# Kernel optimization log

Hardware: AMD Instinct MI355X
Metric: run time of the kernel (lower is better)

## Reference

```python
import jax, jax.numpy as jnp
import numpy as np

N, MUL, NUM_ELEM = 2048, 128, 10
D_IN = 9                      # single-copy input irreps 0e+1o+2e -> 1+3+5
IN_DIMS = (1, 3, 5)           # per-irrep dims of irreps_in
OUT_DIMS = (1, 3)             # per-irrep dims of irreps_out (0e, 1o)
OUT_SLICES = ((0, 1), (1, 4)) # slices into per-mul output of width 4
# (nu, out_idx, n_basis) entries, mirroring reduced_symmetric_tensor_product_basis
ENTRIES = ((1, 0, 1), (1, 1, 1), (2, 0, 3), (2, 1, 2), (3, 0, 4), (3, 1, 2))


def setup_inputs() -> dict:
    key = jax.random.key(0)
    ks = jax.random.split(key, 2 + 2 * len(ENTRIES))
    inp = {}
    inp["node_feats"] = jax.random.normal(ks[0], (N, MUL * D_IN), dtype=jnp.float32)
    inp["species"] = jax.random.randint(ks[1], (N,), 0, NUM_ELEM)
    for i, (nu, oi, nb) in enumerate(ENTRIES):
        d = OUT_DIMS[oi]
        inp[f"basis{i}"] = jax.random.normal(ks[2 + 2 * i], (D_IN,) * nu + (nb, d), dtype=jnp.float32)
        inp[f"weight{i}"] = jax.random.normal(ks[3 + 2 * i], (NUM_ELEM, nb, MUL), dtype=jnp.float32) * (1.0 / np.sqrt(nb))
    return inp


def _to_per_mul(x):
    # (N, sum mul*dim) -> (N, mul, 9)
    pieces, off = [], 0
    for d in IN_DIMS:
        pieces.append(x[:, off:off + MUL * d].reshape(-1, MUL, d))
        off += MUL * d
    return jnp.concatenate(pieces, axis=-1)


def _from_per_mul(x):
    # (N, mul, 4) -> (N, mul*1 + mul*3)
    pieces = []
    for oi, d in enumerate(OUT_DIMS):
        lo, hi = OUT_SLICES[oi]
        pieces.append(x[:, :, lo:hi].reshape(-1, MUL * d))
    return jnp.concatenate(pieces, axis=-1)


def _forward(node_feats, bases, weights, species):
    feats = _to_per_mul(node_feats)                         # (N, mul, 9)
    out = jnp.zeros((feats.shape[0], MUL, 4), dtype=feats.dtype)
    for i, (nu, oi, nb) in enumerate(ENTRIES):
        basis = jax.lax.stop_gradient(bases[i]).astype(feats.dtype)
        tmp = jnp.einsum('a...,nma->nm...', basis, feats)   # (N, mul, 9^(nu-1), nb, d)
        for _ in range(nu - 1):
            tmp = jnp.einsum('nma...,nma->nm...', tmp, feats)
        w = weights[i][species]                             # (N, nb, mul) per-species gather
        contracted = jnp.einsum('nsm,nmsp->nmp', w, tmp)    # (N, mul, d)
        lo, hi = OUT_SLICES[oi]
        out = out.at[:, :, lo:hi].add(contracted)
    return _from_per_mul(out)


def reference(node_feats, species, basis0, weight0, basis1, weight1, basis2, weight2,
              basis3, weight3, basis4, weight4, basis5, weight5):
    bases = [basis0, basis1, basis2, basis3, basis4, basis5]
    weights = [weight0, weight1, weight2, weight3, weight4, weight5]
    return _forward(node_feats, bases, weights, species)
```

## Files before the change

kernel.cpp:

```cpp
#include <hip/hip_runtime.h>


#define N_NODES 2048
#define MUL     128
#define NROW    1152
#define NQ      45
#define NC      165
#define Q4_BASE 12
#define C4_BASE 147
#define S4_TOTAL 642

__global__ void k_prep(const float* __restrict__ b0, const float* __restrict__ b1,
                       const float* __restrict__ b2, const float* __restrict__ b3,
                       const float* __restrict__ b4, const float* __restrict__ b5,
                       float4* __restrict__ S) {
    const int t = threadIdx.x;
    if (t < 9) {
        S[t] = make_float4(b0[t], b1[t * 3 + 0], b1[t * 3 + 1], b1[t * 3 + 2]);
    } else if (t < Q4_BASE) {
        S[t] = make_float4(0.f, 0.f, 0.f, 0.f);
    } else if (t < Q4_BASE + NQ) {
        const int k = t - Q4_BASE;
        int a = -1, b = -1, kk = k;
        for (int aa = 0; aa < 9 && a < 0; ++aa) {
            const int cnt = 9 - aa;
            if (kk < cnt) { a = aa; b = aa + kk; } else kk -= cnt;
        }
        const float mult = (a == b) ? 0.5f : 1.0f;
        const int i1 = a * 9 + b, i2 = b * 9 + a;
        float s2[3], s3[6];
        for (int s = 0; s < 3; ++s)
            s2[s] = (b2[i1 * 3 + s] + b2[i2 * 3 + s]) * mult;
        for (int s = 0; s < 2; ++s)
            for (int d = 0; d < 3; ++d)
                s3[s * 3 + d] = (b3[(i1 * 2 + s) * 3 + d] + b3[(i2 * 2 + s) * 3 + d]) * mult;
        S[Q4_BASE + k * 3 + 0] = make_float4(s2[0], s2[1], s2[2], 0.f);
        S[Q4_BASE + k * 3 + 1] = make_float4(s3[0], s3[1], s3[2], s3[3]);
        S[Q4_BASE + k * 3 + 2] = make_float4(s3[4], s3[5], 0.f, 0.f);
    } else if (t < Q4_BASE + NQ + NC) {
        const int k = t - Q4_BASE - NQ;
        int a = -1, b = -1, c = -1, kk = k;
        for (int aa = 0; aa < 9 && a < 0; ++aa)
            for (int bb = aa; bb < 9 && a < 0; ++bb) {
                const int cnt = 9 - bb;
                if (kk < cnt) { a = aa; b = bb; c = bb + kk; } else kk -= cnt;
            }
        const float mult = (a == b && b == c) ? (1.0f / 6.0f)
                         : ((a == b || b == c) ? 0.5f : 1.0f);
        int p[6];
        p[0] = (a * 9 + b) * 9 + c;  p[1] = (a * 9 + c) * 9 + b;
        p[2] = (b * 9 + a) * 9 + c;  p[3] = (b * 9 + c) * 9 + a;
        p[4] = (c * 9 + a) * 9 + b;  p[5] = (c * 9 + b) * 9 + a;
        float s4[4], s5[6];
        for (int s = 0; s < 4; ++s) {
            float v = 0.f;
            for (int j = 0; j < 6; ++j) v += b4[p[j] * 4 + s];
            s4[s] = v * mult;
        }
        for (int s = 0; s < 2; ++s)
            for (int d = 0; d < 3; ++d) {
                float v = 0.f;
                for (int j = 0; j < 6; ++j) v += b5[(p[j] * 2 + s) * 3 + d];
                s5[s * 3 + d] = v * mult;
            }
        S[C4_BASE + k * 3 + 0] = make_float4(s4[0], s4[1], s4[2], s4[3]);
        S[C4_BASE + k * 3 + 1] = make_float4(s5[0], s5[1], s5[2], s5[3]);
        S[C4_BASE + k * 3 + 2] = make_float4(s5[4], s5[5], 0.f, 0.f);
    }
}

__global__ __launch_bounds__(256) void k_eval(
        const float* __restrict__ nf, const int* __restrict__ species,
        const float* __restrict__ w0, const float* __restrict__ w1,
        const float* __restrict__ w2, const float* __restrict__ w3,
        const float* __restrict__ w4, const float* __restrict__ w5,
        const float4* __restrict__ Sg, float* __restrict__ out) {
    __shared__ float4 S[S4_TOTAL];
    const int tid = threadIdx.x;
    for (int i = tid; i < S4_TOTAL; i += 256) S[i] = Sg[i];
    __syncthreads();

    const int m = tid & 127;
    const int nbase = blockIdx.x * 4 + (tid >> 7) * 2;

    float f[2][9];
    float wv0[2], wv1[2], wv2[2][3], wv3[2][2], wv4[2][4], wv5[2][2];
#pragma unroll
    for (int i = 0; i < 2; ++i) {
        const int n = nbase + i;
        const float* __restrict__ row = nf + (size_t)n * NROW;
        f[i][0] = row[m];
#pragma unroll
        for (int j = 0; j < 3; ++j) f[i][1 + j] = row[128 + 3 * m + j];
#pragma unroll
        for (int j = 0; j < 5; ++j) f[i][4 + j] = row[512 + 5 * m + j];
        const int e = species[n];
        wv0[i] = w0[e * MUL + m];
        wv1[i] = w1[e * MUL + m];
#pragma unroll
        for (int s = 0; s < 3; ++s) wv2[i][s] = w2[(e * 3 + s) * MUL + m];
#pragma unroll
        for (int s = 0; s < 2; ++s) wv3[i][s] = w3[(e * 2 + s) * MUL + m];
#pragma unroll
        for (int s = 0; s < 4; ++s) wv4[i][s] = w4[(e * 4 + s) * MUL + m];
#pragma unroll
        for (int s = 0; s < 2; ++s) wv5[i][s] = w5[(e * 2 + s) * MUL + m];
    }

    float A0[2] = {0.f, 0.f};
    float A1[2][3] = {};
    float B2[2][3] = {}, B3[2][6] = {};
    float B4[2][4] = {}, B5[2][6] = {};

#pragma unroll
    for (int a = 0; a < 9; ++a) {
        const float4 L = S[a];
#pragma unroll
        for (int i = 0; i < 2; ++i) {
            A0[i]    += L.x * f[i][a];
            A1[i][0] += L.y * f[i][a];
            A1[i][1] += L.z * f[i][a];
            A1[i][2] += L.w * f[i][a];
        }
    }

    int kq = 0, kc = 0;
#pragma unroll
    for (int a = 0; a < 9; ++a) {
#pragma unroll
        for (int b = a; b < 9; ++b) {
            float q[2];
            q[0] = f[0][a] * f[0][b];
            q[1] = f[1][a] * f[1][b];
            {
                const float4 r0 = S[Q4_BASE + kq * 3 + 0];
                const float4 r1 = S[Q4_BASE + kq * 3 + 1];
                const float4 r2 = S[Q4_BASE + kq * 3 + 2];
#pragma unroll
                for (int i = 0; i < 2; ++i) {
                    B2[i][0] += q[i] * r0.x; B2[i][1] += q[i] * r0.y; B2[i][2] += q[i] * r0.z;
                    B3[i][0] += q[i] * r1.x; B3[i][1] += q[i] * r1.y; B3[i][2] += q[i] * r1.z;
                    B3[i][3] += q[i] * r1.w; B3[i][4] += q[i] * r2.x; B3[i][5] += q[i] * r2.y;
                }
                ++kq;
            }
#pragma unroll
            for (int c = b; c < 9; ++c) {
                const float4 r0 = S[C4_BASE + kc * 3 + 0];
                const float4 r1 = S[C4_BASE + kc * 3 + 1];
                const float4 r2 = S[C4_BASE + kc * 3 + 2];
#pragma unroll
                for (int i = 0; i < 2; ++i) {
                    const float tt = q[i] * f[i][c];
                    B4[i][0] += tt * r0.x; B4[i][1] += tt * r0.y;
                    B4[i][2] += tt * r0.z; B4[i][3] += tt * r0.w;
                    B5[i][0] += tt * r1.x; B5[i][1] += tt * r1.y; B5[i][2] += tt * r1.z;
                    B5[i][3] += tt * r1.w; B5[i][4] += tt * r2.x; B5[i][5] += tt * r2.y;
                }
                ++kc;
            }
        }
    }

#pragma unroll
    for (int i = 0; i < 2; ++i) {
        const int n = nbase + i;
        float* __restrict__ orow = out + (size_t)n * 512;
        float o0 = wv0[i] * A0[i]
                 + wv2[i][0] * B2[i][0] + wv2[i][1] * B2[i][1] + wv2[i][2] * B2[i][2]
                 + wv4[i][0] * B4[i][0] + wv4[i][1] * B4[i][1]
                 + wv4[i][2] * B4[i][2] + wv4[i][3] * B4[i][3];
        orow[m] = o0;
#pragma unroll
        for (int d = 0; d < 3; ++d) {
            float od = wv1[i] * A1[i][d]
                     + wv3[i][0] * B3[i][d]     + wv3[i][1] * B3[i][3 + d]
                     + wv5[i][0] * B5[i][d]     + wv5[i][1] * B5[i][3 + d];
            orow[128 + 3 * m + d] = od;
        }
    }
}

extern "C" void kernel_launch(void* const* d_in, const int* in_sizes, int n_in,
                              void* d_out, int out_size, void* d_ws, size_t ws_size,
                              hipStream_t stream) {
    const float* nf      = (const float*)d_in[0];
    const int*   species = (const int*)d_in[1];
    const float* b0 = (const float*)d_in[2];  const float* w0 = (const float*)d_in[3];
    const float* b1 = (const float*)d_in[4];  const float* w1 = (const float*)d_in[5];
    const float* b2 = (const float*)d_in[6];  const float* w2 = (const float*)d_in[7];
    const float* b3 = (const float*)d_in[8];  const float* w3 = (const float*)d_in[9];
    const float* b4 = (const float*)d_in[10]; const float* w4 = (const float*)d_in[11];
    const float* b5 = (const float*)d_in[12]; const float* w5 = (const float*)d_in[13];
    float* out = (float*)d_out;

    float4* S = (float4*)d_ws;

    hipLaunchKernelGGL(k_prep, dim3(1), dim3(256), 0, stream,
                       b0, b1, b2, b3, b4, b5, S);
    hipLaunchKernelGGL(k_eval, dim3(512), dim3(256), 0, stream,
                       nf, species, w0, w1, w2, w3, w4, w5,
                       (const float4*)S, out);
}
```

Baseline: 124.2 us.

## Read basis table via constant address space and process one node per thread

```diff
diff --git a/kernel.cpp b/kernel.cpp
--- a/kernel.cpp
+++ b/kernel.cpp
@@ -69,59 +69,55 @@
     }
 }
 
+typedef float fvec4 __attribute__((ext_vector_type(4)));
+
 __global__ __launch_bounds__(256) void k_eval(
         const float* __restrict__ nf, const int* __restrict__ species,
         const float* __restrict__ w0, const float* __restrict__ w1,
         const float* __restrict__ w2, const float* __restrict__ w3,
         const float* __restrict__ w4, const float* __restrict__ w5,
-        const float4* __restrict__ Sg, float* __restrict__ out) {
-    __shared__ float4 S[S4_TOTAL];
+        const float* __restrict__ Sg, float* __restrict__ out) {
+#if defined(__HIP_DEVICE_COMPILE__)
+    typedef const __attribute__((address_space(4))) fvec4* S4cp;
+    S4cp S = (S4cp)(unsigned long long)Sg;
+
     const int tid = threadIdx.x;
-    for (int i = tid; i < S4_TOTAL; i += 256) S[i] = Sg[i];
-    __syncthreads();
+    const int m = tid & 127;
+    const int n = blockIdx.x * 2 + (tid >> 7);
 
-    const int m = tid & 127;
-    const int nbase = blockIdx.x * 4 + (tid >> 7) * 2;
+    const float* __restrict__ row = nf + (size_t)n * NROW;
+    float f[9];
+    f[0] = row[m];
+#pragma unroll
+    for (int j = 0; j < 3; ++j) f[1 + j] = row[128 + 3 * m + j];
+#pragma unroll
+    for (int j = 0; j < 5; ++j) f[4 + j] = row[512 + 5 * m + j];
 
-    float f[2][9];
-    float wv0[2], wv1[2], wv2[2][3], wv3[2][2], wv4[2][4], wv5[2][2];
+    const int e = species[n];
+    const float wv0 = w0[e * MUL + m];
+    const float wv1 = w1[e * MUL + m];
+    float wv2[3], wv3[2], wv4[4], wv5[2];
 #pragma unroll
-    for (int i = 0; i < 2; ++i) {
-        const int n = nbase + i;
-        const float* __restrict__ row = nf + (size_t)n * NROW;
-        f[i][0] = row[m];
+    for (int s = 0; s < 3; ++s) wv2[s] = w2[(e * 3 + s) * MUL + m];
 #pragma unroll
-        for (int j = 0; j < 3; ++j) f[i][1 + j] = row[128 + 3 * m + j];
+    for (int s = 0; s < 2; ++s) wv3[s] = w3[(e * 2 + s) * MUL + m];
 #pragma unroll
-        for (int j = 0; j < 5; ++j) f[i][4 + j] = row[512 + 5 * m + j];
-        const int e = species[n];
-        wv0[i] = w0[e * MUL + m];
-        wv1[i] = w1[e * MUL + m];
+    for (int s = 0; s < 4; ++s) wv4[s] = w4[(e * 4 + s) * MUL + m];
 #pragma unroll
-        for (int s = 0; s < 3; ++s) wv2[i][s] = w2[(e * 3 + s) * MUL + m];
-#pragma unroll
-        for (int s = 0; s < 2; ++s) wv3[i][s] = w3[(e * 2 + s) * MUL + m];
-#pragma unroll
-        for (int s = 0; s < 4; ++s) wv4[i][s] = w4[(e * 4 + s) * MUL + m];
-#pragma unroll
-        for (int s = 0; s < 2; ++s) wv5[i][s] = w5[(e * 2 + s) * MUL + m];
-    }
+    for (int s = 0; s < 2; ++s) wv5[s] = w5[(e * 2 + s) * MUL + m];
 
-    float A0[2] = {0.f, 0.f};
-    float A1[2][3] = {};
-    float B2[2][3] = {}, B3[2][6] = {};
-    float B4[2][4] = {}, B5[2][6] = {};
+    float A0 = 0.f;
+    float A1[3] = {};
+    float B2[3] = {}, B3[6] = {};
+    float B4[4] = {}, B5[6] = {};
 
 #pragma unroll
     for (int a = 0; a < 9; ++a) {
-        const float4 L = S[a];
-#pragma unroll
-        for (int i = 0; i < 2; ++i) {
-            A0[i]    += L.x * f[i][a];
-            A1[i][0] += L.y * f[i][a];
-            A1[i][1] += L.z * f[i][a];
-            A1[i][2] += L.w * f[i][a];
-        }
+        const fvec4 L = S[a];
+        A0    += L.x * f[a];
+        A1[0] += L.y * f[a];
+        A1[1] += L.z * f[a];
+        A1[2] += L.w * f[a];
     }
 
     int kq = 0, kc = 0;
@@ -129,56 +125,42 @@
     for (int a = 0; a < 9; ++a) {
 #pragma unroll
         for (int b = a; b < 9; ++b) {
-            float q[2];
-            q[0] = f[0][a] * f[0][b];
-            q[1] = f[1][a] * f[1][b];
+            const float q = f[a] * f[b];
             {
-                const float4 r0 = S[Q4_BASE + kq * 3 + 0];
-                const float4 r1 = S[Q4_BASE + kq * 3 + 1];
-                const float4 r2 = S[Q4_BASE + kq * 3 + 2];
-#pragma unroll
-                for (int i = 0; i < 2; ++i) {
-                    B2[i][0] += q[i] * r0.x; B2[i][1] += q[i] * r0.y; B2[i][2] += q[i] * r0.z;
-                    B3[i][0] += q[i] * r1.x; B3[i][1] += q[i] * r1.y; B3[i][2] += q[i] * r1.z;
-                    B3[i][3] += q[i] * r1.w; B3[i][4] += q[i] * r2.x; B3[i][5] += q[i] * r2.y;
-                }
+                const fvec4 r0 = S[Q4_BASE + kq * 3 + 0];
+                const fvec4 r1 = S[Q4_BASE + kq * 3 + 1];
+                const fvec4 r2 = S[Q4_BASE + kq * 3 + 2];
+                B2[0] += q * r0.x; B2[1] += q * r0.y; B2[2] += q * r0.z;
+                B3[0] += q * r1.x; B3[1] += q * r1.y; B3[2] += q * r1.z;
+                B3[3] += q * r1.w; B3[4] += q * r2.x; B3[5] += q * r2.y;
                 ++kq;
             }
 #pragma unroll
             for (int c = b; c < 9; ++c) {
-                const float4 r0 = S[C4_BASE + kc * 3 + 0];
-                const float4 r1 = S[C4_BASE + kc * 3 + 1];
-                const float4 r2 = S[C4_BASE + kc * 3 + 2];
-#pragma unroll
-                for (int i = 0; i < 2; ++i) {
-                    const float tt = q[i] * f[i][c];
-                    B4[i][0] += tt * r0.x; B4[i][1] += tt * r0.y;
-                    B4[i][2] += tt * r0.z; B4[i][3] += tt * r0.w;
-                    B5[i][0] += tt * r1.x; B5[i][1] += tt * r1.y; B5[i][2] += tt * r1.z;
-                    B5[i][3] += tt * r1.w; B5[i][4] += tt * r2.x; B5[i][5] += tt * r2.y;
-                }
+                const fvec4 r0 = S[C4_BASE + kc * 3 + 0];
+                const fvec4 r1 = S[C4_BASE + kc * 3 + 1];
+                const fvec4 r2 = S[C4_BASE + kc * 3 + 2];
+                const float tt = q * f[c];
+                B4[0] += tt * r0.x; B4[1] += tt * r0.y;
+                B4[2] += tt * r0.z; B4[3] += tt * r0.w;
+                B5[0] += tt * r1.x; B5[1] += tt * r1.y; B5[2] += tt * r1.z;
+                B5[3] += tt * r1.w; B5[4] += tt * r2.x; B5[5] += tt * r2.y;
                 ++kc;
             }
         }
     }
 
+    float* __restrict__ orow = out + (size_t)n * 512;
+    orow[m] = wv0 * A0
+            + wv2[0] * B2[0] + wv2[1] * B2[1] + wv2[2] * B2[2]
+            + wv4[0] * B4[0] + wv4[1] * B4[1] + wv4[2] * B4[2] + wv4[3] * B4[3];
 #pragma unroll
-    for (int i = 0; i < 2; ++i) {
-        const int n = nbase + i;
-        float* __restrict__ orow = out + (size_t)n * 512;
-        float o0 = wv0[i] * A0[i]
-                 + wv2[i][0] * B2[i][0] + wv2[i][1] * B2[i][1] + wv2[i][2] * B2[i][2]
-                 + wv4[i][0] * B4[i][0] + wv4[i][1] * B4[i][1]
-                 + wv4[i][2] * B4[i][2] + wv4[i][3] * B4[i][3];
-        orow[m] = o0;
-#pragma unroll
-        for (int d = 0; d < 3; ++d) {
-            float od = wv1[i] * A1[i][d]
-                     + wv3[i][0] * B3[i][d]     + wv3[i][1] * B3[i][3 + d]
-                     + wv5[i][0] * B5[i][d]     + wv5[i][1] * B5[i][3 + d];
-            orow[128 + 3 * m + d] = od;
-        }
+    for (int d = 0; d < 3; ++d) {
+        orow[128 + 3 * m + d] = wv1 * A1[d]
+                              + wv3[0] * B3[d] + wv3[1] * B3[3 + d]
+                              + wv5[0] * B5[d] + wv5[1] * B5[3 + d];
     }
+#endif
 }
 
 extern "C" void kernel_launch(void* const* d_in, const int* in_sizes, int n_in,
@@ -198,7 +180,7 @@
 
     hipLaunchKernelGGL(k_prep, dim3(1), dim3(256), 0, stream,
                        b0, b1, b2, b3, b4, b5, S);
-    hipLaunchKernelGGL(k_eval, dim3(512), dim3(256), 0, stream,
+    hipLaunchKernelGGL(k_eval, dim3(1024), dim3(256), 0, stream,
                        nf, species, w0, w1, w2, w3, w4, w5,
-                       (const float4*)S, out);
+                       (const float*)S, out);
 }
```

New measurement: 114.0 us. -8.2%, faster.

## Split cubic contraction across warp groups with shared-memory reduction and constant-space basis

Applied to the files above, without the earlier changes.

```diff
diff --git a/kernel.cpp b/kernel.cpp
--- a/kernel.cpp
+++ b/kernel.cpp
@@ -6,6 +6,8 @@
 #define NROW    1152
 #define NQ      45
 #define NC      165
+#define KC1     55
+#define KC2     110
 #define Q4_BASE 12
 #define C4_BASE 147
 #define S4_TOTAL 642
@@ -69,116 +71,165 @@
     }
 }
 
-__global__ __launch_bounds__(256) void k_eval(
+typedef float fvec4 __attribute__((ext_vector_type(4)));
+
+#if defined(__HIP_DEVICE_COMPILE__)
+typedef const __attribute__((address_space(4))) fvec4* S4cp;
+
+template<int LO, int HI>
+__device__ __forceinline__ void do_cubics(S4cp S, const float (&f)[4][9],
+                                          float (&B4)[4][4], float (&B5)[4][6]) {
+    int kc = 0;
+#pragma unroll
+    for (int a = 0; a < 9; ++a) {
+#pragma unroll
+        for (int b = a; b < 9; ++b) {
+            float q[4];
+#pragma unroll
+            for (int i = 0; i < 4; ++i) q[i] = f[i][a] * f[i][b];
+#pragma unroll
+            for (int c = b; c < 9; ++c) {
+                if (kc >= LO && kc < HI) {
+                    const fvec4 r0 = S[C4_BASE + kc * 3 + 0];
+                    const fvec4 r1 = S[C4_BASE + kc * 3 + 1];
+                    const fvec4 r2 = S[C4_BASE + kc * 3 + 2];
+#pragma unroll
+                    for (int i = 0; i < 4; ++i) {
+                        const float tt = q[i] * f[i][c];
+                        B4[i][0] += tt * r0.x; B4[i][1] += tt * r0.y;
+                        B4[i][2] += tt * r0.z; B4[i][3] += tt * r0.w;
+                        B5[i][0] += tt * r1.x; B5[i][1] += tt * r1.y;
+                        B5[i][2] += tt * r1.z; B5[i][3] += tt * r1.w;
+                        B5[i][4] += tt * r2.x; B5[i][5] += tt * r2.y;
+                    }
+                }
+                ++kc;
+            }
+        }
+    }
+}
+#endif
+
+__global__ __launch_bounds__(512, 4) void k_eval(
         const float* __restrict__ nf, const int* __restrict__ species,
         const float* __restrict__ w0, const float* __restrict__ w1,
         const float* __restrict__ w2, const float* __restrict__ w3,
         const float* __restrict__ w4, const float* __restrict__ w5,
-        const float4* __restrict__ Sg, float* __restrict__ out) {
-    __shared__ float4 S[S4_TOTAL];
-    const int tid = threadIdx.x;
-    for (int i = tid; i < S4_TOTAL; i += 256) S[i] = Sg[i];
-    __syncthreads();
-
-    const int m = tid & 127;
-    const int nbase = blockIdx.x * 4 + (tid >> 7) * 2;
-
-    float f[2][9];
-    float wv0[2], wv1[2], wv2[2][3], wv3[2][2], wv4[2][4], wv5[2][2];
-#pragma unroll
-    for (int i = 0; i < 2; ++i) {
-        const int n = nbase + i;
-        const float* __restrict__ row = nf + (size_t)n * NROW;
+        const float* __restrict__ Sg, float* __restrict__ out) {
+#if defined(__HIP_DEVICE_COMPILE__)
+    S4cp S = (S4cp)(unsigned long long)Sg;
+
+    __shared__ float red[3][MUL][4][12];
+
+    const int tid  = threadIdx.x;
+    const int m    = tid & 127;
+    const int part = tid >> 7;
+    const int nb   = blockIdx.x * 4;
+
+    float f[4][9];
+#pragma unroll
+    for (int i = 0; i < 4; ++i) {
+        const float* __restrict__ row = nf + (size_t)(nb + i) * NROW;
         f[i][0] = row[m];
 #pragma unroll
         for (int j = 0; j < 3; ++j) f[i][1 + j] = row[128 + 3 * m + j];
 #pragma unroll
         for (int j = 0; j < 5; ++j) f[i][4 + j] = row[512 + 5 * m + j];
-        const int e = species[n];
-        wv0[i] = w0[e * MUL + m];
-        wv1[i] = w1[e * MUL + m];
-#pragma unroll
-        for (int s = 0; s < 3; ++s) wv2[i][s] = w2[(e * 3 + s) * MUL + m];
-#pragma unroll
-        for (int s = 0; s < 2; ++s) wv3[i][s] = w3[(e * 2 + s) * MUL + m];
-#pragma unroll
-        for (int s = 0; s < 4; ++s) wv4[i][s] = w4[(e * 4 + s) * MUL + m];
-#pragma unroll
-        for (int s = 0; s < 2; ++s) wv5[i][s] = w5[(e * 2 + s) * MUL + m];
-    }
-
-    float A0[2] = {0.f, 0.f};
-    float A1[2][3] = {};
-    float B2[2][3] = {}, B3[2][6] = {};
-    float B4[2][4] = {}, B5[2][6] = {};
-
-#pragma unroll
-    for (int a = 0; a < 9; ++a) {
-        const float4 L = S[a];
-#pragma unroll
-        for (int i = 0; i < 2; ++i) {
-            A0[i]    += L.x * f[i][a];
-            A1[i][0] += L.y * f[i][a];
-            A1[i][1] += L.z * f[i][a];
-            A1[i][2] += L.w * f[i][a];
-        }
-    }
-
-    int kq = 0, kc = 0;
-#pragma unroll
-    for (int a = 0; a < 9; ++a) {
-#pragma unroll
-        for (int b = a; b < 9; ++b) {
-            float q[2];
-            q[0] = f[0][a] * f[0][b];
-            q[1] = f[1][a] * f[1][b];
-            {
-                const float4 r0 = S[Q4_BASE + kq * 3 + 0];
-                const float4 r1 = S[Q4_BASE + kq * 3 + 1];
-                const float4 r2 = S[Q4_BASE + kq * 3 + 2];
-#pragma unroll
-                for (int i = 0; i < 2; ++i) {
-                    B2[i][0] += q[i] * r0.x; B2[i][1] += q[i] * r0.y; B2[i][2] += q[i] * r0.z;
-                    B3[i][0] += q[i] * r1.x; B3[i][1] += q[i] * r1.y; B3[i][2] += q[i] * r1.z;
-                    B3[i][3] += q[i] * r1.w; B3[i][4] += q[i] * r2.x; B3[i][5] += q[i] * r2.y;
+    }
+
+    float A0[4] = {}, A1[4][3] = {};
+    float B2[4][3] = {}, B3[4][6] = {};
+    float B4[4][4] = {}, B5[4][6] = {};
+    float wv0[4], wv1[4], wv2[4][3], wv3[4][2], wv4[4][4], wv5[4][2];
+
+    if (part == 0) {
+#pragma unroll
+        for (int a = 0; a < 9; ++a) {
+            const fvec4 L = S[a];
+#pragma unroll
+            for (int i = 0; i < 4; ++i) {
+                A0[i]    += L.x * f[i][a];
+                A1[i][0] += L.y * f[i][a];
+                A1[i][1] += L.z * f[i][a];
+                A1[i][2] += L.w * f[i][a];
+            }
+        }
+        int kq = 0;
+#pragma unroll
+        for (int a = 0; a < 9; ++a) {
+#pragma unroll
+            for (int b = a; b < 9; ++b) {
+                const fvec4 r0 = S[Q4_BASE + kq * 3 + 0];
+                const fvec4 r1 = S[Q4_BASE + kq * 3 + 1];
+                const fvec4 r2 = S[Q4_BASE + kq * 3 + 2];
+#pragma unroll
+                for (int i = 0; i < 4; ++i) {
+                    const float q = f[i][a] * f[i][b];
+                    B2[i][0] += q * r0.x; B2[i][1] += q * r0.y; B2[i][2] += q * r0.z;
+                    B3[i][0] += q * r1.x; B3[i][1] += q * r1.y; B3[i][2] += q * r1.z;
+                    B3[i][3] += q * r1.w; B3[i][4] += q * r2.x; B3[i][5] += q * r2.y;
                 }
                 ++kq;
             }
-#pragma unroll
-            for (int c = b; c < 9; ++c) {
-                const float4 r0 = S[C4_BASE + kc * 3 + 0];
-                const float4 r1 = S[C4_BASE + kc * 3 + 1];
-                const float4 r2 = S[C4_BASE + kc * 3 + 2];
-#pragma unroll
-                for (int i = 0; i < 2; ++i) {
-                    const float tt = q[i] * f[i][c];
-                    B4[i][0] += tt * r0.x; B4[i][1] += tt * r0.y;
-                    B4[i][2] += tt * r0.z; B4[i][3] += tt * r0.w;
-                    B5[i][0] += tt * r1.x; B5[i][1] += tt * r1.y; B5[i][2] += tt * r1.z;
-                    B5[i][3] += tt * r1.w; B5[i][4] += tt * r2.x; B5[i][5] += tt * r2.y;
-                }
-                ++kc;
-            }
-        }
-    }
-
-#pragma unroll
-    for (int i = 0; i < 2; ++i) {
-        const int n = nbase + i;
-        float* __restrict__ orow = out + (size_t)n * 512;
-        float o0 = wv0[i] * A0[i]
-                 + wv2[i][0] * B2[i][0] + wv2[i][1] * B2[i][1] + wv2[i][2] * B2[i][2]
-                 + wv4[i][0] * B4[i][0] + wv4[i][1] * B4[i][1]
-                 + wv4[i][2] * B4[i][2] + wv4[i][3] * B4[i][3];
-        orow[m] = o0;
-#pragma unroll
-        for (int d = 0; d < 3; ++d) {
-            float od = wv1[i] * A1[i][d]
-                     + wv3[i][0] * B3[i][d]     + wv3[i][1] * B3[i][3 + d]
-                     + wv5[i][0] * B5[i][d]     + wv5[i][1] * B5[i][3 + d];
-            orow[128 + 3 * m + d] = od;
-        }
-    }
+        }
+#pragma unroll
+        for (int i = 0; i < 4; ++i) {
+            const int e = species[nb + i];
+            wv0[i] = w0[e * MUL + m];
+            wv1[i] = w1[e * MUL + m];
+#pragma unroll
+            for (int s = 0; s < 3; ++s) wv2[i][s] = w2[(e * 3 + s) * MUL + m];
+#pragma unroll
+            for (int s = 0; s < 2; ++s) wv3[i][s] = w3[(e * 2 + s) * MUL + m];
+#pragma unroll
+            for (int s = 0; s < 4; ++s) wv4[i][s] = w4[(e * 4 + s) * MUL + m];
+#pragma unroll
+            for (int s = 0; s < 2; ++s) wv5[i][s] = w5[(e * 2 + s) * MUL + m];
+        }
+    } else {
+        if (part == 1)      do_cubics<0,   KC1>(S, f, B4, B5);
+        else if (part == 2) do_cubics<KC1, KC2>(S, f, B4, B5);
+        else                do_cubics<KC2, NC >(S, f, B4, B5);
+        float* __restrict__ dst = &red[part - 1][m][0][0];
+#pragma unroll
+        for (int i = 0; i < 4; ++i) {
+#pragma unroll
+            for (int j = 0; j < 4; ++j) dst[i * 12 + j] = B4[i][j];
+#pragma unroll
+            for (int j = 0; j < 6; ++j) dst[i * 12 + 4 + j] = B5[i][j];
+        }
+    }
+
+    __syncthreads();
+
+    if (part == 0) {
+#pragma unroll
+        for (int p = 0; p < 3; ++p) {
+            const float* __restrict__ src = &red[p][m][0][0];
+#pragma unroll
+            for (int i = 0; i < 4; ++i) {
+#pragma unroll
+                for (int j = 0; j < 4; ++j) B4[i][j] += src[i * 12 + j];
+#pragma unroll
+                for (int j = 0; j < 6; ++j) B5[i][j] += src[i * 12 + 4 + j];
+            }
+        }
+#pragma unroll
+        for (int i = 0; i < 4; ++i) {
+            float* __restrict__ orow = out + (size_t)(nb + i) * 512;
+            orow[m] = wv0[i] * A0[i]
+                    + wv2[i][0] * B2[i][0] + wv2[i][1] * B2[i][1] + wv2[i][2] * B2[i][2]
+                    + wv4[i][0] * B4[i][0] + wv4[i][1] * B4[i][1]
+                    + wv4[i][2] * B4[i][2] + wv4[i][3] * B4[i][3];
+#pragma unroll
+            for (int d = 0; d < 3; ++d) {
+                orow[128 + 3 * m + d] = wv1[i] * A1[i][d]
+                                      + wv3[i][0] * B3[i][d] + wv3[i][1] * B3[i][3 + d]
+                                      + wv5[i][0] * B5[i][d] + wv5[i][1] * B5[i][3 + d];
+            }
+        }
+    }
+#endif
 }
 
 extern "C" void kernel_launch(void* const* d_in, const int* in_sizes, int n_in,
@@ -198,7 +249,7 @@
 
     hipLaunchKernelGGL(k_prep, dim3(1), dim3(256), 0, stream,
                        b0, b1, b2, b3, b4, b5, S);
-    hipLaunchKernelGGL(k_eval, dim3(512), dim3(256), 0, stream,
+    hipLaunchKernelGGL(k_eval, dim3(N_NODES / 4), dim3(512), 0, stream,
                        nf, species, w0, w1, w2, w3, w4, w5,
-                       (const float4*)S, out);
-}
+                       (const float*)S, out);
+}
```

New measurement: 144.5 us. 16.3% more time.
